# Performance work log

Hardware: AMD Instinct MI355X
Metric: run time of the kernel (lower is better)

The kernel has to match this reference:

```python
import jax, jax.numpy as jnp
import numpy as np

BATCH = 2
SEQ = 2048
DIM = 2048
HEADS = 16
DIM_HEAD = 64
DIM_INNER = HEADS * DIM_HEAD  # 1024
SOFTCAP = 50.0
EPS = 1e-12


def setup_inputs() -> dict:
    key = jax.random.key(0)
    k1, k2, k3, k4 = jax.random.split(key, 4)
    x = jax.random.normal(k1, (BATCH, SEQ, DIM), dtype=jnp.float32)
    # RMSNorm gamma param (initialized near zero in the torch module)
    gamma = jax.random.normal(k2, (DIM,), dtype=jnp.float32) * 0.02
    # Linear weights stored already-transposed: x @ W
    w_qkv = jax.random.normal(k3, (DIM, 3 * DIM_INNER), dtype=jnp.float32) * (DIM ** -0.5)
    w_out = jax.random.normal(k4, (DIM_INNER, DIM), dtype=jnp.float32) * (DIM_INNER ** -0.5)
    # (type, offset, length) triples per batch; bidirectional attention inside each span
    modalities = jnp.array(
        [[[0, 256, 256], [0, 1024, 512]],
         [[0, 128, 256], [0, 1536, 384]]], dtype=jnp.int32)
    return dict(x=x, gamma=gamma, w_qkv=w_qkv, w_out=w_out, modalities=modalities)


def _transfusion_attn_mask(seq_len, modalities):
    # causal | (q in span AND kv in span)  -> Bool[b, i, j]
    seq = jnp.arange(seq_len)
    causal = seq[:, None] >= seq[None, :]                      # [i, j]
    offsets = modalities[..., 1]                                # [b, m]
    ends = offsets + modalities[..., 2]                         # [b, m]
    q_in = seq[None, None, :] >= offsets[..., None]             # [b, m, i]
    kv_in = seq[None, None, :] < ends[..., None]                # [b, m, j]
    is_modality = jnp.any(q_in[..., :, None] & kv_in[..., None, :], axis=1)  # [b, i, j]
    return causal[None] | is_modality


def _rmsnorm(x, gamma):
    n = jnp.sqrt(jnp.sum(x * x, axis=-1, keepdims=True))
    x = x / jnp.maximum(n, EPS)
    return x * (DIM ** 0.5) * (gamma + 1.0)


def reference(x, gamma, w_qkv, w_out, modalities):
    xn = _rmsnorm(x, gamma)
    qkv = xn @ w_qkv                                            # [b, n, 3*h*d]
    qkv = qkv.reshape(BATCH, SEQ, 3, HEADS, DIM_HEAD)
    qkv = jnp.transpose(qkv, (2, 0, 3, 1, 4))                   # [3, b, h, n, d]
    q, k, v = qkv[0], qkv[1], qkv[2]
    q = q * (DIM_HEAD ** -0.5)
    sim = jnp.einsum('bhid,bhjd->bhij', q, k)
    sim = jnp.tanh(sim / SOFTCAP) * SOFTCAP                     # softclamp
    mask = _transfusion_attn_mask(SEQ, modalities)              # [b, i, j]
    neg = -jnp.finfo(sim.dtype).max
    sim = jnp.where(mask[:, None, :, :], sim, neg)
    attn = jax.nn.softmax(sim, axis=-1)
    out = jnp.einsum('bhij,bhjd->bhid', attn, v)
    out = jnp.transpose(out, (0, 2, 1, 3)).reshape(BATCH, SEQ, DIM_INNER)
    return out @ w_out
```

## Files before the change

kernel.cpp:

```cpp
#include <hip/hip_runtime.h>
#include <hip/hip_bf16.h>

typedef unsigned short u16;
typedef unsigned int u32;
typedef __attribute__((ext_vector_type(8))) short short8;
typedef __attribute__((ext_vector_type(4))) float f32x4;
typedef __attribute__((ext_vector_type(4))) u16 u16x4;

#define DEV __device__ __forceinline__

DEV u16 f2bf(float f) {
    union { float f; u32 u; } v; v.f = f;
    u32 r = v.u;
    u32 lsb = (r >> 16) & 1u;
    r += 0x7fffu + lsb;
    return (u16)(r >> 16);
}

DEV void gload_lds16(const u16* g, u16* l) {
    __builtin_amdgcn_global_load_lds(
        (const __attribute__((address_space(1))) u32*)(const void*)g,
        (__attribute__((address_space(3))) u32*)(void*)l,
        16, 0, 0);
}

__global__ void prep(const float* __restrict__ x, const float* __restrict__ gamma,
                     const float* __restrict__ w_qkv, const float* __restrict__ w_out,
                     u16* __restrict__ xn, u16* __restrict__ wqkvT, u16* __restrict__ woutT) {
    __shared__ float tile[32][33];
    __shared__ float red[4];
    int id = blockIdx.x;
    int t = threadIdx.x;
    if (id < 8192) {
        const float* in; u16* out; int R, C, bx, by;
        if (id < 6144) { in = w_qkv; out = wqkvT; R = 2048; C = 3072; bx = id % 96; by = id / 96; }
        else { id -= 6144; in = w_out; out = woutT; R = 1024; C = 2048; bx = id % 64; by = id / 64; }
        int tx = t & 31, ty = t >> 5;
        int c0 = bx * 32, r0 = by * 32;
#pragma unroll
        for (int i = 0; i < 4; i++)
            tile[ty * 4 + i][tx] = in[(size_t)(r0 + ty * 4 + i) * C + c0 + tx];
        __syncthreads();
#pragma unroll
        for (int i = 0; i < 4; i++)
            out[(size_t)(c0 + ty * 4 + i) * R + r0 + tx] = f2bf(tile[tx][ty * 4 + i]);
    } else {
        int row = id - 8192;
        const float4* xr = (const float4*)(x + (size_t)row * 2048);
        float4 a = xr[t];
        float4 b = xr[256 + t];
        float ss = a.x * a.x + a.y * a.y + a.z * a.z + a.w * a.w +
                   b.x * b.x + b.y * b.y + b.z * b.z + b.w * b.w;
#pragma unroll
        for (int off = 32; off; off >>= 1) ss += __shfl_xor(ss, off);
        if ((t & 63) == 0) red[t >> 6] = ss;
        __syncthreads();
        float tot = red[0] + red[1] + red[2] + red[3];
        float n = sqrtf(tot);
        float inv = 45.254833995939045f / fmaxf(n, 1e-12f);
        const float4* gr = (const float4*)gamma;
        float4 g0 = gr[t], g1 = gr[256 + t];
        u16x4 o0 = { f2bf(a.x * inv * (g0.x + 1.f)), f2bf(a.y * inv * (g0.y + 1.f)),
                     f2bf(a.z * inv * (g0.z + 1.f)), f2bf(a.w * inv * (g0.w + 1.f)) };
        u16x4 o1 = { f2bf(b.x * inv * (g1.x + 1.f)), f2bf(b.y * inv * (g1.y + 1.f)),
                     f2bf(b.z * inv * (g1.z + 1.f)), f2bf(b.w * inv * (g1.w + 1.f)) };
        u16x4* xo = (u16x4*)(xn + (size_t)row * 2048);
        xo[t] = o0;
        xo[256 + t] = o1;
    }
}

template <int EPI, int CCOL>
__global__ __launch_bounds__(512, 1) void gemmpp(
    const u16* __restrict__ A, const u16* __restrict__ BT,
    int M, int N, int K,
    float* __restrict__ Cout,
    u16* __restrict__ qb, u16* __restrict__ kb, u16* __restrict__ vT) {
    __shared__ __align__(16) u16 As[2][2][8192];
    __shared__ __align__(16) u16 Bs[2][2][8192];
    int t = threadIdx.x, lane = t & 63, wid = t >> 6;
    int g = lane >> 4, r = lane & 15;
    int wm = wid >> 2, wn = wid & 3;
    int rsw = r & 7;

    int id = blockIdx.x;
    int xcd = id & 7, slot = id >> 3;
    int by = (xcd >> 1) * 4 + slot / CCOL;
    int bx = (xcd & 1) * CCOL + slot % CCOL;
    int brow = by * 256, bcol = bx * 256;

    int gsl = (t & 7) ^ ((t >> 3) & 7);
    const u16* AgH = A + (size_t)(brow + (t >> 3)) * K + gsl * 8;
    const u16* BgH = BT + (size_t)(bcol + (t >> 3)) * K + gsl * 8;
    const size_t loK = (size_t)128 * K, r64K = (size_t)64 * K;
    int dstc = t * 8;

    f32x4 acc[2][4][2][2] = {};
    short8 a0[4][2], a1[4][2], b0[2][2], b1[2][2];
    int NT = K >> 6;

#define STG_AH(bf_, kt_) { gload_lds16(AgH + (kt_) * 64, &As[bf_][0][dstc]); \
                           gload_lds16(AgH + r64K + (kt_) * 64, &As[bf_][0][dstc + 4096]); }
#define STG_AL(bf_, kt_) { gload_lds16(AgH + loK + (kt_) * 64, &As[bf_][1][dstc]); \
                           gload_lds16(AgH + loK + r64K + (kt_) * 64, &As[bf_][1][dstc + 4096]); }
#define STG_BH(bf_, kt_) { gload_lds16(BgH + (kt_) * 64, &Bs[bf_][0][dstc]); \
                           gload_lds16(BgH + r64K + (kt_) * 64, &Bs[bf_][0][dstc + 4096]); }
#define STG_BL(bf_, kt_) { gload_lds16(BgH + loK + (kt_) * 64, &Bs[bf_][1][dstc]); \
                           gload_lds16(BgH + loK + r64K + (kt_) * 64, &Bs[bf_][1][dstc + 4096]); }
#define RD_A(dst_, bb_, hh_) { \
    _Pragma("unroll") for (int mf = 0; mf < 4; mf++) \
    _Pragma("unroll") for (int ks = 0; ks < 2; ks++) \
        dst_[mf][ks] = *(const short8*)&As[bb_][hh_][(wm * 64 + mf * 16 + r) * 64 + (((ks << 2) + g) ^ rsw) * 8]; }
#define RD_B(dst_, bb_, hh_) { \
    _Pragma("unroll") for (int nf = 0; nf < 2; nf++) \
    _Pragma("unroll") for (int ks = 0; ks < 2; ks++) \
        dst_[nf][ks] = *(const short8*)&Bs[bb_][hh_][(wn * 32 + nf * 16 + r) * 64 + (((ks << 2) + g) ^ rsw) * 8]; }
#define MFMA_Q(qm_, qn_, aa_, bb_) { \
    __builtin_amdgcn_s_setprio(1); \
    _Pragma("unroll") for (int ks = 0; ks < 2; ks++) \
    _Pragma("unroll") for (int mf = 0; mf < 4; mf++) \
    _Pragma("unroll") for (int nf = 0; nf < 2; nf++) \
        acc[qm_][mf][qn_][nf] = __builtin_amdgcn_mfma_f32_16x16x32_bf16( \
            aa_[mf][ks], bb_[nf][ks], acc[qm_][mf][qn_][nf], 0, 0, 0); \
    __builtin_amdgcn_s_setprio(0); }
#define SCHEDB() __builtin_amdgcn_sched_barrier(0)
#define BAR() __builtin_amdgcn_s_barrier()

    STG_AH(0, 0); STG_AL(0, 0); STG_BH(0, 0); STG_BL(0, 0);
    if (NT > 1) { STG_AH(1, 1); STG_AL(1, 1); STG_BH(1, 1); }
    asm volatile("s_waitcnt vmcnt(6)" ::: "memory");
    SCHEDB();
    BAR();
    RD_A(a0, 0, 0);
    RD_B(b0, 0, 0);

    for (int kt = 0; kt < NT; ++kt) {
        int buf = kt & 1, ob = buf ^ 1;
        bool s1 = kt + 1 < NT, s2 = kt + 2 < NT;

        RD_B(b1, buf, 1);
        if (s1) STG_BL(ob, kt + 1);
        asm volatile("s_waitcnt lgkmcnt(4)" ::: "memory");
        SCHEDB();
        MFMA_Q(0, 0, a0, b0);
        BAR();

        RD_A(a1, buf, 1);
        if (s2) STG_AH(buf, kt + 2);
        asm volatile("s_waitcnt lgkmcnt(8)" ::: "memory");
        SCHEDB();
        MFMA_Q(0, 1, a0, b1);
        BAR();

        asm volatile("s_waitcnt lgkmcnt(0)" ::: "memory");
        SCHEDB();
        MFMA_Q(1, 0, a1, b0);
        BAR();

        if (s2) { STG_AL(buf, kt + 2); STG_BH(buf, kt + 2); }
        if (s2)      { asm volatile("s_waitcnt vmcnt(6)" ::: "memory"); }
        else if (s1) { asm volatile("s_waitcnt vmcnt(0)" ::: "memory"); }
        SCHEDB();
        if (s1) { RD_A(a0, ob, 0); RD_B(b0, ob, 0); }
        MFMA_Q(1, 1, a1, b1);
        BAR();
    }
#undef STG_AH
#undef STG_AL
#undef STG_BH
#undef STG_BL
#undef RD_A
#undef RD_B
#undef MFMA_Q
#undef SCHEDB
#undef BAR

    if (EPI == 0) {
#pragma unroll
        for (int qm = 0; qm < 2; qm++)
#pragma unroll
            for (int mf = 0; mf < 4; mf++)
#pragma unroll
                for (int qn = 0; qn < 2; qn++)
#pragma unroll
                    for (int nf = 0; nf < 2; nf++) {
                        int cb = bcol + qn * 128 + wn * 32 + nf * 16 + r;
                        int which = cb >> 10;
                        int hd = cb & 1023;
                        int hh = hd >> 6, d = hd & 63;
#pragma unroll
                        for (int j = 0; j < 4; j++) {
                            int rr = brow + qm * 128 + wm * 64 + mf * 16 + 4 * g + j;
                            int b = rr >> 11, nn = rr & 2047;
                            float v = acc[qm][mf][qn][nf][j];
                            size_t bh = (size_t)(b * 16 + hh);
                            if (which == 0)      qb[(bh * 2048 + nn) * 64 + d] = f2bf(v * 0.125f);
                            else if (which == 1) kb[(bh * 2048 + nn) * 64 + d] = f2bf(v);
                            else                 vT[(bh * 64 + d) * 2048 + nn] = f2bf(v);
                        }
                    }
    } else {
#pragma unroll
        for (int qm = 0; qm < 2; qm++)
#pragma unroll
            for (int mf = 0; mf < 4; mf++)
#pragma unroll
                for (int qn = 0; qn < 2; qn++)
#pragma unroll
                    for (int nf = 0; nf < 2; nf++) {
                        int cb = bcol + qn * 128 + wn * 32 + nf * 16 + r;
#pragma unroll
                        for (int j = 0; j < 4; j++) {
                            int rr = brow + qm * 128 + wm * 64 + mf * 16 + 4 * g + j;
                            Cout[(size_t)rr * N + cb] = acc[qm][mf][qn][nf][j];
                        }
                    }
    }
}

__global__ __launch_bounds__(256, 3) void flash_attn(
    const u16* __restrict__ q, const u16* __restrict__ kk, const u16* __restrict__ vT,
    const int* __restrict__ mods, u16* __restrict__ attn_out) {
    __shared__ __align__(16) u16 Ks[2][4096];
    __shared__ __align__(16) u16 Vs[2][4096];
    __shared__ __align__(16) u16 Plds[4][16][72];
    int t = threadIdx.x, lane = t & 63, wave = t >> 6;
    int g = lane >> 4, r = lane & 15;
    int h = blockIdx.x, b = blockIdx.y;
    int qs = (31 - blockIdx.z) * 64;
    int bh = b * 16 + h;
    int qbase = qs + wave * 16;

    int off0 = mods[b * 6 + 1], end0 = off0 + mods[b * 6 + 2];
    int off1 = mods[b * 6 + 4], end1 = off1 + mods[b * 6 + 5];

    const u16* Qp = q + ((size_t)bh * 2048 + qbase) * 64;
    short8 qf0 = *(const short8*)(Qp + (size_t)r * 64 + 8 * g);
    short8 qf1 = *(const short8*)(Qp + (size_t)r * 64 + 32 + 8 * g);

    int iq = qbase + r;
    int lim0 = (iq >= off0) ? end0 : 0;
    int lim1 = (iq >= off1) ? end1 : 0;
    int rowlim = max(iq + 1, max(lim0, lim1));

    int jlb = qs + 64;
    if (qs + 63 >= off0) jlb = max(jlb, end0);
    if (qs + 63 >= off1) jlb = max(jlb, end1);

    const u16* Kp = kk + (size_t)bh * 2048 * 64;
    const u16* Vp = vT + (size_t)bh * 64 * 2048;
    u16* Pw = &Plds[wave][0][0];

    f32x4 ot[4] = {};
    float psA = 0.f, psB = 0.f;
    int sw = r & 7;

    auto stage64 = [&](const u16* gbase, int gstride, u16* lds) {
#pragma unroll
        for (int i = 0; i < 2; i++) {
            int c = i * 256 + t;
            int row = c >> 3;
            int gsl = (c & 7) ^ (row & 7);
            gload_lds16(gbase + (size_t)row * gstride + 8 * gsl,
                        lds + (size_t)(c & ~63) * 8);
        }
    };

    stage64(Kp, 64, Ks[0]);
    stage64(Vp, 2048, Vs[0]);
    int buf = 0;

    for (int jb = 0; jb < jlb; jb += 64) {
        if (jb + 64 < jlb) {
            stage64(Kp + (size_t)(jb + 64) * 64, 64, Ks[buf ^ 1]);
            stage64(Vp + (jb + 64), 2048, Vs[buf ^ 1]);
            asm volatile("s_waitcnt vmcnt(4)" ::: "memory");
        } else {
            asm volatile("s_waitcnt vmcnt(0)" ::: "memory");
        }
        __builtin_amdgcn_s_barrier();
        const u16* Kt = Ks[buf];
        const u16* Vt = Vs[buf];

        f32x4 st[4];
#pragma unroll
        for (int tt = 0; tt < 4; tt++) {
            int row = 16 * tt + r;
            short8 kf0 = *(const short8*)&Kt[(size_t)(row * 8 + (g ^ sw)) * 8];
            short8 kf1 = *(const short8*)&Kt[(size_t)(row * 8 + ((4 + g) ^ sw)) * 8];
            f32x4 z = {};
            z = __builtin_amdgcn_mfma_f32_16x16x32_bf16(kf0, qf0, z, 0, 0, 0);
            z = __builtin_amdgcn_mfma_f32_16x16x32_bf16(kf1, qf1, z, 0, 0, 0);
            st[tt] = z;
        }
#pragma unroll
        for (int tt = 0; tt < 4; tt++) {
            int kvb = jb + 16 * tt + 4 * g;
            float p0, p1, p2, p3;
#pragma unroll
            for (int j = 0; j < 4; j++) {
                float x = st[tt][j];
                float x2 = x * x;
                float inner = __builtin_fmaf(x2, 2.1333333e-8f, -1.3333333e-4f);
                float poly = __builtin_fmaf(x2, inner, 1.0f);
                float pv = __expf(x * poly);
                pv = (kvb + j < rowlim) ? pv : 0.f;
                if (j == 0) p0 = pv; else if (j == 1) p1 = pv;
                else if (j == 2) p2 = pv; else p3 = pv;
            }
            psA += p0 + p1;
            psB += p2 + p3;
            u32 pk0, pk1;
            asm("v_cvt_pk_bf16_f32 %0, %1, %2" : "=v"(pk0) : "v"(p0), "v"(p1));
            asm("v_cvt_pk_bf16_f32 %0, %1, %2" : "=v"(pk1) : "v"(p2), "v"(p3));
            *(u32*)&Pw[r * 72 + 16 * tt + 4 * g] = pk0;
            *(u32*)&Pw[r * 72 + 16 * tt + 4 * g + 2] = pk1;
        }
        short8 pf0 = *(const short8*)&Pw[r * 72 + 8 * g];
        short8 pf1 = *(const short8*)&Pw[r * 72 + 32 + 8 * g];
#pragma unroll
        for (int dt = 0; dt < 4; dt++) {
            int row = 16 * dt + r;
            short8 vf0 = *(const short8*)&Vt[(size_t)(row * 8 + (g ^ sw)) * 8];
            short8 vf1 = *(const short8*)&Vt[(size_t)(row * 8 + ((4 + g) ^ sw)) * 8];
            ot[dt] = __builtin_amdgcn_mfma_f32_16x16x32_bf16(vf0, pf0, ot[dt], 0, 0, 0);
            ot[dt] = __builtin_amdgcn_mfma_f32_16x16x32_bf16(vf1, pf1, ot[dt], 0, 0, 0);
        }
        asm volatile("s_waitcnt lgkmcnt(0)" ::: "memory");
        __builtin_amdgcn_s_barrier();
        buf ^= 1;
    }

    float lrow = psA + psB;
    lrow += __shfl_xor(lrow, 16);
    lrow += __shfl_xor(lrow, 32);
    float inv = 1.f / lrow;
    u16* Op = attn_out + ((size_t)(b * 2048 + qbase + r)) * 1024 + h * 64;
#pragma unroll
    for (int dt = 0; dt < 4; dt++) {
        u16x4 o = { f2bf(ot[dt][0] * inv), f2bf(ot[dt][1] * inv),
                    f2bf(ot[dt][2] * inv), f2bf(ot[dt][3] * inv) };
        *(u16x4*)(Op + dt * 16 + 4 * g) = o;
    }
}

extern "C" void kernel_launch(void* const* d_in, const int* in_sizes, int n_in,
                              void* d_out, int out_size, void* d_ws, size_t ws_size,
                              hipStream_t stream) {
    const float* x = (const float*)d_in[0];
    const float* gamma = (const float*)d_in[1];
    const float* w_qkv = (const float*)d_in[2];
    const float* w_out = (const float*)d_in[3];
    const int* mods = (const int*)d_in[4];
    float* out = (float*)d_out;

    u16* ws = (u16*)d_ws;
    u16* xn    = ws;
    u16* wqkvT = ws + 8388608;
    u16* woutT = ws + 14680064;
    u16* qb    = ws + 16777216;
    u16* kb    = ws + 20971520;
    u16* vT    = ws + 25165824;
    u16* ao    = ws + 29360128;

    prep<<<dim3(12288), dim3(256), 0, stream>>>(x, gamma, w_qkv, w_out, xn, wqkvT, woutT);
    gemmpp<0, 6><<<dim3(192), dim3(512), 0, stream>>>(xn, wqkvT, 4096, 3072, 2048,
                                                      nullptr, qb, kb, vT);
    flash_attn<<<dim3(16, 2, 32), dim3(256), 0, stream>>>(qb, kb, vT, mods, ao);
    gemmpp<1, 4><<<dim3(128), dim3(512), 0, stream>>>(ao, woutT, 4096, 2048, 1024,
                                                      out, nullptr, nullptr, nullptr);
}
```

Before: 189.4 us.

## Narrow GEMM N-tile to fill all CUs and restructure K-loop schedule

Templates the GEMM on the N-tile width, using 192 columns for the QKV projection and 128 for the output projection. Both launches now use 256 blocks instead of 192/128, so every CU on the device gets a tile. The K loop is rescheduled: one B register set is shared across both M halves, A halves are reloaded per half, and global-to-LDS staging is interleaved between MFMA groups. Narrower tiles reuse each A load across fewer columns, so global and LDS traffic per FLOP goes up, and the new wait counts and barriers could expose latency.

```diff
diff --git a/kernel.cpp b/kernel.cpp
--- a/kernel.cpp
+++ b/kernel.cpp
@@ -70,108 +70,107 @@
     }
 }
 
-template <int EPI, int CCOL>
-__global__ __launch_bounds__(512, 1) void gemmpp(
+template <int EPI, int BN, int CCOL>
+__global__ __launch_bounds__(512, 1) void gemmcf(
     const u16* __restrict__ A, const u16* __restrict__ BT,
     int M, int N, int K,
     float* __restrict__ Cout,
     u16* __restrict__ qb, u16* __restrict__ kb, u16* __restrict__ vT) {
+    constexpr int HN = BN / 2;
+    constexpr int NF2 = BN / 64;
+    constexpr int NG0 = (NF2 + 1) / 2;
+    constexpr bool B2 = (HN * 8) > 512;
     __shared__ __align__(16) u16 As[2][2][8192];
-    __shared__ __align__(16) u16 Bs[2][2][8192];
+    __shared__ __align__(16) u16 Bs[2][2][HN * 64];
     int t = threadIdx.x, lane = t & 63, wid = t >> 6;
     int g = lane >> 4, r = lane & 15;
     int wm = wid >> 2, wn = wid & 3;
+    int bhalf = wn >> 1;
+    int cb0w = (wn & 1) * (BN / 4);
     int rsw = r & 7;
 
     int id = blockIdx.x;
     int xcd = id & 7, slot = id >> 3;
     int by = (xcd >> 1) * 4 + slot / CCOL;
     int bx = (xcd & 1) * CCOL + slot % CCOL;
-    int brow = by * 256, bcol = bx * 256;
+    int brow = by * 256, bcol = bx * BN;
 
     int gsl = (t & 7) ^ ((t >> 3) & 7);
-    const u16* AgH = A + (size_t)(brow + (t >> 3)) * K + gsl * 8;
-    const u16* BgH = BT + (size_t)(bcol + (t >> 3)) * K + gsl * 8;
-    const size_t loK = (size_t)128 * K, r64K = (size_t)64 * K;
+    const u16* Ag = A + (size_t)(brow + (t >> 3)) * K + gsl * 8;
+    const u16* Bg = BT + (size_t)(bcol + (t >> 3)) * K + gsl * 8;
     int dstc = t * 8;
 
-    f32x4 acc[2][4][2][2] = {};
-    short8 a0[4][2], a1[4][2], b0[2][2], b1[2][2];
+    f32x4 acc[2][4][NF2] = {};
+    short8 areg[4][2], breg[NF2][2];
     int NT = K >> 6;
 
-#define STG_AH(bf_, kt_) { gload_lds16(AgH + (kt_) * 64, &As[bf_][0][dstc]); \
-                           gload_lds16(AgH + r64K + (kt_) * 64, &As[bf_][0][dstc + 4096]); }
-#define STG_AL(bf_, kt_) { gload_lds16(AgH + loK + (kt_) * 64, &As[bf_][1][dstc]); \
-                           gload_lds16(AgH + loK + r64K + (kt_) * 64, &As[bf_][1][dstc + 4096]); }
-#define STG_BH(bf_, kt_) { gload_lds16(BgH + (kt_) * 64, &Bs[bf_][0][dstc]); \
-                           gload_lds16(BgH + r64K + (kt_) * 64, &Bs[bf_][0][dstc + 4096]); }
-#define STG_BL(bf_, kt_) { gload_lds16(BgH + loK + (kt_) * 64, &Bs[bf_][1][dstc]); \
-                           gload_lds16(BgH + loK + r64K + (kt_) * 64, &Bs[bf_][1][dstc + 4096]); }
-#define RD_A(dst_, bb_, hh_) { \
+#define STG_A(bf_, kt_, h_) { \
+        gload_lds16(Ag + (size_t)((h_) * 128) * K + (kt_) * 64, &As[bf_][h_][dstc]); \
+        gload_lds16(Ag + (size_t)((h_) * 128 + 64) * K + (kt_) * 64, &As[bf_][h_][4096 + dstc]); }
+#define STG_B(bf_, kt_, h_) { \
+        gload_lds16(Bg + (size_t)((h_) * HN) * K + (kt_) * 64, &Bs[bf_][h_][dstc]); \
+        if constexpr (B2) { if (t < 256) \
+            gload_lds16(Bg + (size_t)((h_) * HN + 64) * K + (kt_) * 64, &Bs[bf_][h_][4096 + dstc]); } }
+#define RD_A(qm_) { \
     _Pragma("unroll") for (int mf = 0; mf < 4; mf++) \
     _Pragma("unroll") for (int ks = 0; ks < 2; ks++) \
-        dst_[mf][ks] = *(const short8*)&As[bb_][hh_][(wm * 64 + mf * 16 + r) * 64 + (((ks << 2) + g) ^ rsw) * 8]; }
-#define RD_B(dst_, bb_, hh_) { \
-    _Pragma("unroll") for (int nf = 0; nf < 2; nf++) \
+        areg[mf][ks] = *(const short8*)&As[buf][qm_][(wm * 64 + mf * 16 + r) * 64 + (((ks << 2) + g) ^ rsw) * 8]; }
+#define RD_B() { \
+    _Pragma("unroll") for (int nf = 0; nf < NF2; nf++) \
     _Pragma("unroll") for (int ks = 0; ks < 2; ks++) \
-        dst_[nf][ks] = *(const short8*)&Bs[bb_][hh_][(wn * 32 + nf * 16 + r) * 64 + (((ks << 2) + g) ^ rsw) * 8]; }
-#define MFMA_Q(qm_, qn_, aa_, bb_) { \
+        breg[nf][ks] = *(const short8*)&Bs[buf][bhalf][(cb0w + nf * 16 + r) * 64 + (((ks << 2) + g) ^ rsw) * 8]; }
+#define MFMA_G(qm_, nf0_, nf1_) { \
     __builtin_amdgcn_s_setprio(1); \
     _Pragma("unroll") for (int ks = 0; ks < 2; ks++) \
     _Pragma("unroll") for (int mf = 0; mf < 4; mf++) \
-    _Pragma("unroll") for (int nf = 0; nf < 2; nf++) \
-        acc[qm_][mf][qn_][nf] = __builtin_amdgcn_mfma_f32_16x16x32_bf16( \
-            aa_[mf][ks], bb_[nf][ks], acc[qm_][mf][qn_][nf], 0, 0, 0); \
+    _Pragma("unroll") for (int nf = nf0_; nf < nf1_; nf++) \
+        acc[qm_][mf][nf] = __builtin_amdgcn_mfma_f32_16x16x32_bf16( \
+            areg[mf][ks], breg[nf][ks], acc[qm_][mf][nf], 0, 0, 0); \
     __builtin_amdgcn_s_setprio(0); }
 #define SCHEDB() __builtin_amdgcn_sched_barrier(0)
 #define BAR() __builtin_amdgcn_s_barrier()
 
-    STG_AH(0, 0); STG_AL(0, 0); STG_BH(0, 0); STG_BL(0, 0);
-    if (NT > 1) { STG_AH(1, 1); STG_AL(1, 1); STG_BH(1, 1); }
-    asm volatile("s_waitcnt vmcnt(6)" ::: "memory");
+    STG_A(0, 0, 0); STG_A(0, 0, 1); STG_B(0, 0, 0); STG_B(0, 0, 1);
+    if (NT > 1) { STG_A(1, 1, 0); STG_A(1, 1, 1); }
+    if (NT > 1) { asm volatile("s_waitcnt vmcnt(4)" ::: "memory"); }
+    else        { asm volatile("s_waitcnt vmcnt(0)" ::: "memory"); }
     SCHEDB();
     BAR();
-    RD_A(a0, 0, 0);
-    RD_B(b0, 0, 0);
 
     for (int kt = 0; kt < NT; ++kt) {
         int buf = kt & 1, ob = buf ^ 1;
         bool s1 = kt + 1 < NT, s2 = kt + 2 < NT;
 
-        RD_B(b1, buf, 1);
-        if (s1) STG_BL(ob, kt + 1);
-        asm volatile("s_waitcnt lgkmcnt(4)" ::: "memory");
-        SCHEDB();
-        MFMA_Q(0, 0, a0, b0);
-        BAR();
-
-        RD_A(a1, buf, 1);
-        if (s2) STG_AH(buf, kt + 2);
-        asm volatile("s_waitcnt lgkmcnt(8)" ::: "memory");
-        SCHEDB();
-        MFMA_Q(0, 1, a0, b1);
-        BAR();
-
+        RD_B(); RD_A(0);
+        if (s1) STG_B(ob, kt + 1, 1);
         asm volatile("s_waitcnt lgkmcnt(0)" ::: "memory");
         SCHEDB();
-        MFMA_Q(1, 0, a1, b0);
+        MFMA_G(0, 0, NG0);
         BAR();
 
-        if (s2) { STG_AL(buf, kt + 2); STG_BH(buf, kt + 2); }
-        if (s2)      { asm volatile("s_waitcnt vmcnt(6)" ::: "memory"); }
+        if (s1) STG_B(ob, kt + 1, 0);
+        if (s2) STG_A(buf, kt + 2, 0);
+        MFMA_G(0, NG0, NF2);
+        BAR();
+
+        RD_A(1);
+        asm volatile("s_waitcnt lgkmcnt(0)" ::: "memory");
+        SCHEDB();
+        MFMA_G(1, 0, NG0);
+        BAR();
+
+        if (s2) STG_A(buf, kt + 2, 1);
+        MFMA_G(1, NG0, NF2);
+        if (s2)      { asm volatile("s_waitcnt vmcnt(4)" ::: "memory"); }
         else if (s1) { asm volatile("s_waitcnt vmcnt(0)" ::: "memory"); }
         SCHEDB();
-        if (s1) { RD_A(a0, ob, 0); RD_B(b0, ob, 0); }
-        MFMA_Q(1, 1, a1, b1);
         BAR();
     }
-#undef STG_AH
-#undef STG_AL
-#undef STG_BH
-#undef STG_BL
+#undef STG_A
+#undef STG_B
 #undef RD_A
 #undef RD_B
-#undef MFMA_Q
+#undef MFMA_G
 #undef SCHEDB
 #undef BAR
 
@@ -181,40 +180,36 @@
 #pragma unroll
             for (int mf = 0; mf < 4; mf++)
 #pragma unroll
-                for (int qn = 0; qn < 2; qn++)
-#pragma unroll
-                    for (int nf = 0; nf < 2; nf++) {
-                        int cb = bcol + qn * 128 + wn * 32 + nf * 16 + r;
-                        int which = cb >> 10;
-                        int hd = cb & 1023;
-                        int hh = hd >> 6, d = hd & 63;
-#pragma unroll
-                        for (int j = 0; j < 4; j++) {
-                            int rr = brow + qm * 128 + wm * 64 + mf * 16 + 4 * g + j;
-                            int b = rr >> 11, nn = rr & 2047;
-                            float v = acc[qm][mf][qn][nf][j];
-                            size_t bh = (size_t)(b * 16 + hh);
-                            if (which == 0)      qb[(bh * 2048 + nn) * 64 + d] = f2bf(v * 0.125f);
-                            else if (which == 1) kb[(bh * 2048 + nn) * 64 + d] = f2bf(v);
-                            else                 vT[(bh * 64 + d) * 2048 + nn] = f2bf(v);
-                        }
+                for (int nf = 0; nf < NF2; nf++) {
+                    int cb = bcol + bhalf * HN + cb0w + nf * 16 + r;
+                    int which = cb >> 10;
+                    int hd = cb & 1023;
+                    int hh = hd >> 6, d = hd & 63;
+#pragma unroll
+                    for (int j = 0; j < 4; j++) {
+                        int rr = brow + qm * 128 + wm * 64 + mf * 16 + 4 * g + j;
+                        int b = rr >> 11, nn = rr & 2047;
+                        float v = acc[qm][mf][nf][j];
+                        size_t bh = (size_t)(b * 16 + hh);
+                        if (which == 0)      qb[(bh * 2048 + nn) * 64 + d] = f2bf(v * 0.125f);
+                        else if (which == 1) kb[(bh * 2048 + nn) * 64 + d] = f2bf(v);
+                        else                 vT[(bh * 64 + d) * 2048 + nn] = f2bf(v);
                     }
+                }
     } else {
 #pragma unroll
         for (int qm = 0; qm < 2; qm++)
 #pragma unroll
             for (int mf = 0; mf < 4; mf++)
 #pragma unroll
-                for (int qn = 0; qn < 2; qn++)
-#pragma unroll
-                    for (int nf = 0; nf < 2; nf++) {
-                        int cb = bcol + qn * 128 + wn * 32 + nf * 16 + r;
-#pragma unroll
-                        for (int j = 0; j < 4; j++) {
-                            int rr = brow + qm * 128 + wm * 64 + mf * 16 + 4 * g + j;
-                            Cout[(size_t)rr * N + cb] = acc[qm][mf][qn][nf][j];
-                        }
+                for (int nf = 0; nf < NF2; nf++) {
+                    int cb = bcol + bhalf * HN + cb0w + nf * 16 + r;
+#pragma unroll
+                    for (int j = 0; j < 4; j++) {
+                        int rr = brow + qm * 128 + wm * 64 + mf * 16 + 4 * g + j;
+                        Cout[(size_t)rr * N + cb] = acc[qm][mf][nf][j];
                     }
+                }
     }
 }
 
@@ -364,9 +359,9 @@
     u16* ao    = ws + 29360128;
 
     prep<<<dim3(12288), dim3(256), 0, stream>>>(x, gamma, w_qkv, w_out, xn, wqkvT, woutT);
-    gemmpp<0, 6><<<dim3(192), dim3(512), 0, stream>>>(xn, wqkvT, 4096, 3072, 2048,
-                                                      nullptr, qb, kb, vT);
+    gemmcf<0, 192, 8><<<dim3(256), dim3(512), 0, stream>>>(xn, wqkvT, 4096, 3072, 2048,
+                                                           nullptr, qb, kb, vT);
     flash_attn<<<dim3(16, 2, 32), dim3(256), 0, stream>>>(qb, kb, vT, mods, ao);
-    gemmpp<1, 4><<<dim3(128), dim3(512), 0, stream>>>(ao, woutT, 4096, 2048, 1024,
-                                                      out, nullptr, nullptr, nullptr);
-}
+    gemmcf<1, 128, 8><<<dim3(256), dim3(512), 0, stream>>>(ao, woutT, 4096, 2048, 1024,
+                                                           out, nullptr, nullptr, nullptr);
+}
```

Measured after the change: 164.1 us. -13.4%, faster.
